# Kernel optimization log

Measured on AMD Instinct MI355X. Metric: run time of the kernel, lower is better.

The kernel has to match this reference:

```python
import jax, jax.numpy as jnp
import numpy as np

RADIUS = 1.3
RES = 256
N_INT = 128
STEP = 0.02


def grid_sample3d(grid, coords):
    # grid: [C, D, H, W]; coords: [N, 3] as (x, y, z) in [-1, 1]
    # trilinear, align_corners=True, border clamp (torch grid_sample semantics)
    D, H, W = grid.shape[1], grid.shape[2], grid.shape[3]

    def to_idx(c, size):
        return jnp.clip((c + 1.0) * 0.5 * (size - 1), 0.0, size - 1.0)

    x = to_idx(coords[:, 0], W)
    y = to_idx(coords[:, 1], H)
    z = to_idx(coords[:, 2], D)
    x0 = jnp.floor(x).astype(jnp.int32)
    y0 = jnp.floor(y).astype(jnp.int32)
    z0 = jnp.floor(z).astype(jnp.int32)
    x1 = jnp.minimum(x0 + 1, W - 1)
    y1 = jnp.minimum(y0 + 1, H - 1)
    z1 = jnp.minimum(z0 + 1, D - 1)
    wx = x - x0.astype(x.dtype)
    wy = y - y0.astype(y.dtype)
    wz = z - z0.astype(z.dtype)

    def g(zi, yi, xi):
        return grid[:, zi, yi, xi]  # [C, N]

    c00 = g(z0, y0, x0) * (1 - wx) + g(z0, y0, x1) * wx
    c01 = g(z0, y1, x0) * (1 - wx) + g(z0, y1, x1) * wx
    c10 = g(z1, y0, x0) * (1 - wx) + g(z1, y0, x1) * wx
    c11 = g(z1, y1, x0) * (1 - wx) + g(z1, y1, x1) * wx
    c0 = c00 * (1 - wy) + c01 * wy
    c1 = c10 * (1 - wy) + c11 * wy
    return (c0 * (1 - wz) + c1 * wz).T  # [N, C]


def sh16(d):
    # real spherical harmonics, degree 4 (instant-ngp / tcnn convention), d unit
    x, y, z = d[:, 0], d[:, 1], d[:, 2]
    xx, yy, zz = x * x, y * y, z * z
    xy, yz, xz = x * y, y * z, x * z
    return jnp.stack([
        jnp.full_like(x, 0.28209479177387814),
        -0.48860251190291987 * y,
        0.48860251190291987 * z,
        -0.48860251190291987 * x,
        1.0925484305920792 * xy,
        -1.0925484305920792 * yz,
        0.94617469575755997 * zz - 0.31539156525251999,
        -1.0925484305920792 * xz,
        0.54627421529603959 * (xx - yy),
        0.59004358992664352 * y * (-3.0 * xx + yy),
        2.8906114426405538 * xy * z,
        0.45704579946446572 * y * (1.0 - 5.0 * zz),
        0.3731763325901154 * z * (5.0 * zz - 3.0),
        0.45704579946446572 * x * (1.0 - 5.0 * zz),
        1.445305721320277 * z * (xx - yy),
        0.59004358992664352 * x * (-xx + 3.0 * yy),
    ], axis=-1)  # [N, 16]


def mlp3(x, W0, W1, W2):
    # FullyFusedMLP: no bias, ReLU hidden, linear output
    h = jnp.maximum(x @ W0, 0.0)
    h = jnp.maximum(h @ W1, 0.0)
    return h @ W2


def setup_inputs() -> dict:
    key = jax.random.key(0)
    k = jax.random.split(key, 10)
    B, FD, NF = 4096, 32, 16
    rays_o = jax.random.normal(k[0], (B, 3), jnp.float32) * 0.5
    rays_d = jax.random.normal(k[1], (B, 3), jnp.float32)
    G1 = jax.random.normal(k[2], (3, RES, RES, RES), jnp.float32) * 0.02
    F = jax.random.normal(k[3], (FD, NF, NF, NF), jnp.float32) * 0.05
    W_sig0 = jax.random.normal(k[4], (FD, 128), jnp.float32) / np.sqrt(FD).astype(np.float32)
    W_sig1 = jax.random.normal(k[5], (128, 128), jnp.float32) / np.float32(np.sqrt(128))
    W_sig2 = jax.random.normal(k[6], (128, 16), jnp.float32) / np.float32(np.sqrt(128))
    W_col0 = jax.random.normal(k[7], (31, 64), jnp.float32) / np.float32(np.sqrt(31))
    W_col1 = jax.random.normal(k[8], (64, 64), jnp.float32) / np.float32(np.sqrt(64))
    W_col2 = jax.random.normal(k[9], (64, 3), jnp.float32) / np.float32(np.sqrt(64))
    return {"rays_o": rays_o, "rays_d": rays_d, "G1": G1, "F": F,
            "W_sig0": W_sig0, "W_sig1": W_sig1, "W_sig2": W_sig2,
            "W_col0": W_col0, "W_col1": W_col1, "W_col2": W_col2}


def reference(rays_o, rays_d, G1, F, W_sig0, W_sig1, W_sig2, W_col0, W_col1, W_col2):
    B = rays_o.shape[0]
    d = rays_d / jnp.linalg.norm(rays_d, axis=-1, keepdims=True)
    # ray-sphere intersection |o + t d| = RADIUS (unit d)
    b = jnp.sum(rays_o * d, axis=-1)
    c = jnp.sum(rays_o * rays_o, axis=-1) - RADIUS ** 2
    disc = b * b - c
    hit = disc > 0
    s = jnp.sqrt(jnp.where(hit, disc, 1.0))
    tmin = jnp.where(hit, jnp.maximum(-b - s, 0.0), 0.0)
    tmax = jnp.where(hit, -b + s, 0.0)
    t = tmin[:, None] + jnp.arange(N_INT + 1, dtype=jnp.float32)[None, :] * STEP  # [B, n+1]
    tmid = 0.5 * (t[:, :-1] + t[:, 1:])  # [B, n]
    mask = hit[:, None] & (tmid <= tmax[:, None])  # [B, n]
    pts = rays_o[:, None, :] + d[:, None, :] * tmid[..., None]  # [B, n, 3]
    coords = (pts / RADIUS).reshape(-1, 3)  # in [-1, 1]
    # hash/indirection lookup: G1 gives learned coords into feature grid F
    g1 = grid_sample3d(G1, coords)        # [N, 3]
    feats = grid_sample3d(F, g1)          # [N, 32]
    sig_out = mlp3(feats, W_sig0, W_sig1, W_sig2)  # [N, 16]
    sigma = jnp.where(mask, sig_out[:, 0].reshape(B, N_INT), 0.0)
    sigma = jnp.maximum(sigma, 0.0)
    pd = jnp.broadcast_to(d[:, None, :], (B, N_INT, 3)).reshape(-1, 3)
    enc = sh16(pd)
    col_raw = mlp3(jnp.concatenate([enc, sig_out[:, 1:]], axis=-1), W_col0, W_col1, W_col2)
    col = jnp.where(mask[..., None], col_raw.reshape(B, N_INT, 3), 0.0)
    # volume rendering (sigma2alpha + shrgb2rgb with white background)
    alpha = 1.0 - jnp.exp(-sigma * STEP)
    T = jnp.cumprod(1.0 - alpha + 1e-10, axis=1)
    T_excl = jnp.concatenate([jnp.ones((B, 1), alpha.dtype), T[:, :-1]], axis=1)
    w = alpha * T_excl
    rgb = jnp.einsum('bn,bnc->bc', w, jax.nn.sigmoid(col))
    rgb = rgb + (1.0 - jnp.sum(w, axis=1, keepdims=True))
    return rgb
```

## Files before the change

kernel.cpp:

```cpp
#include <hip/hip_runtime.h>
#include <stdint.h>

#define STEP 0.02f
#define INV_RADIUS (1.0f/1.3f)
#define RADIUS 1.3f

typedef __bf16   bf16x8 __attribute__((ext_vector_type(8)));
typedef float    f32x4  __attribute__((ext_vector_type(4)));
typedef uint32_t u32x4  __attribute__((ext_vector_type(4)));
typedef uint32_t u32x4a __attribute__((ext_vector_type(4), aligned(8)));

#define FT_OFF   0
#define W0_OFF   262144
#define W1_OFF   270336
#define W2_OFF   303104
#define C0_OFF   307200
#define C1_OFF   311296
#define C2_OFF   319488
#define G1T_OFF  321536
#define WS_NEED  (321536ull + 134217728ull)

#define FE_BYTES  4096
#define SIG_OFF   8192
#define COL_OFF   8704
#define BLOCK_LDS 10752

__device__ __forceinline__ uint32_t pack2(float a, float b){
    uint32_t ua = __float_as_uint(a); ua += 0x7FFFu + ((ua>>16)&1u);
    uint32_t ub = __float_as_uint(b); ub += 0x7FFFu + ((ub>>16)&1u);
    return (ua>>16) | (ub & 0xFFFF0000u);
}
__device__ __forceinline__ float bfl(uint32_t u){ return __uint_as_float(u << 16); }
__device__ __forceinline__ float bfh(uint32_t u){ return __uint_as_float(u & 0xFFFF0000u); }
__device__ __forceinline__ void toidx(float c, float sizem1, int isize,
                                      int& i0, int& i1, float& w){
    float t = (c + 1.f) * 0.5f * sizem1;
    t = fminf(fmaxf(t, 0.f), sizem1);
    float f = floorf(t);
    i0 = (int)f;
    i1 = i0 + 1; if (i1 > isize - 1) i1 = isize - 1;
    w = t - f;
}
__device__ __forceinline__ void lds_fence(){
    asm volatile("s_waitcnt lgkmcnt(0)" ::: "memory");
}
__device__ __forceinline__ uint32_t cvtpk(float lo, float hi){
    uint32_t r;
    asm("v_cvt_pk_bf16_f32 %0, %1, %2" : "=v"(r) : "v"(lo), "v"(hi));
    return r;
}
__device__ __forceinline__ void p32swap(uint32_t& a, uint32_t& b){
    asm("v_permlane32_swap_b32 %0, %1" : "+v"(a), "+v"(b));
}
__device__ __forceinline__ void p16swap(uint32_t& a, uint32_t& b){
    asm("v_permlane16_swap_b32 %0, %1" : "+v"(a), "+v"(b));
}
__device__ __forceinline__ uint32_t pkrelu(float a, float b){
    return cvtpk(fmaxf(a, 0.f), fmaxf(b, 0.f));
}
__device__ __forceinline__ bf16x8 frag_from(uint32_t a, uint32_t b, uint32_t c, uint32_t d){
    union { u32x4 u; bf16x8 h; } cv;
    cv.u = (u32x4){a, b, c, d};
    return cv.h;
}
__device__ __forceinline__ bf16x8 xpose4(const f32x4& t0, const f32x4& t1){
    uint32_t A = pkrelu(t0[0], t0[1]);
    uint32_t B = pkrelu(t0[2], t0[3]);
    uint32_t C = pkrelu(t1[0], t1[1]);
    uint32_t D = pkrelu(t1[2], t1[3]);
    p32swap(A, C); p16swap(A, C);
    p32swap(B, D); p16swap(B, D);
    return frag_from(A, B, C, D);
}
__device__ __forceinline__ void rowlerp(const u32x4a d, bool xe, float wx,
                                        float& v0, float& v1, float& v2){
    uint32_t a01 = xe ? d[2] : d[0];
    uint32_t a2w = xe ? d[3] : d[1];
    float a0 = bfl(a01), a1 = bfh(a01), a2 = bfl(a2w);
    float b0 = bfl(d[2]), b1 = bfh(d[2]), b2 = bfl(d[3]);
    v0 = a0 + (b0 - a0)*wx;
    v1 = a1 + (b1 - a1)*wx;
    v2 = a2 + (b2 - a2)*wx;
}

__global__ __launch_bounds__(256) void prep_g1(const float* __restrict__ G1, uint32_t* __restrict__ dst){
    int idx2 = (blockIdx.x*256 + threadIdx.x)*2;
    float2 a = *(const float2*)(G1 + idx2);
    float2 b = *(const float2*)(G1 + idx2 + 16777216);
    float2 c = *(const float2*)(G1 + idx2 + 33554432);
    uint4 o = make_uint4(pack2(a.x, b.x), pack2(c.x, 0.f),
                         pack2(a.y, b.y), pack2(c.y, 0.f));
    *(uint4*)(dst + idx2*2) = o;
}

__global__ __launch_bounds__(256) void prep_f(const float* __restrict__ F, uint32_t* __restrict__ ws){
    int idx = blockIdx.x * 256 + threadIdx.x;
    if (idx >= 4096) return;
    uint32_t o[16];
    #pragma unroll
    for (int c = 0; c < 16; c++){
        float a = F[(2*c  )*4096 + idx];
        float b = F[(2*c+1)*4096 + idx];
        o[c] = pack2(a, b);
    }
    uint4* dst = (uint4*)ws;
    #pragma unroll
    for (int q = 0; q < 4; q++)
        dst[idx*4 + q] = make_uint4(o[q*4], o[q*4+1], o[q*4+2], o[q*4+3]);
}

__global__ __launch_bounds__(256) void prep_w(const float* __restrict__ W0, const float* __restrict__ W1,
                                              const float* __restrict__ W2, const float* __restrict__ Wc0,
                                              const float* __restrict__ Wc1, const float* __restrict__ Wc2,
                                              char* __restrict__ ws){
    int gid = blockIdx.x * 256 + threadIdx.x;
    if (gid >= 58*64) return;
    int cg = gid >> 6, lane = gid & 63;
    const float* src; int K, N, base_cg, dstoff;
    if      (cg < 8)  { src = W0;  K = 32;  N = 128; base_cg = 0;  dstoff = W0_OFF; }
    else if (cg < 40) { src = W1;  K = 128; N = 128; base_cg = 8;  dstoff = W1_OFF; }
    else if (cg < 44) { src = W2;  K = 128; N = 16;  base_cg = 40; dstoff = W2_OFF; }
    else if (cg < 48) { src = Wc0; K = 31;  N = 64;  base_cg = 44; dstoff = C0_OFF; }
    else if (cg < 56) { src = Wc1; K = 64;  N = 64;  base_cg = 48; dstoff = C1_OFF; }
    else              { src = Wc2; K = 64;  N = 3;   base_cg = 56; dstoff = C2_OFF; }
    bool c0remap = (cg >= 44 && cg < 48);
    int local = cg - base_cg;
    int NT = (N + 15) >> 4;
    int nt = local % NT, kk = local / NT;
    int n = nt*16 + (lane & 15);
    int kbase = kk*32 + (lane >> 4)*8;
    uint32_t o[4];
    #pragma unroll
    for (int jj = 0; jj < 4; jj++){
        int k0 = kbase + jj*2, k1 = k0 + 1;
        int k0s = (c0remap && k0 > 16) ? k0 - 1 : k0;
        int k1s = (c0remap && k1 > 16) ? k1 - 1 : k1;
        bool v0 = (n < N) && (k0s < K) && !(c0remap && k0 == 16);
        bool v1 = (n < N) && (k1s < K) && !(c0remap && k1 == 16);
        float a = v0 ? src[k0s*N + n] : 0.f;
        float b = v1 ? src[k1s*N + n] : 0.f;
        o[jj] = pack2(a, b);
    }
    uint4* dst = (uint4*)(ws + dstoff);
    dst[local*64 + lane] = make_uint4(o[0], o[1], o[2], o[3]);
}

template<bool G1PACK>
__global__ __launch_bounds__(128, 2)
void nerf_fused(const float* __restrict__ rays_o, const float* __restrict__ rays_d,
                const float* __restrict__ G1, const char* __restrict__ ws,
                float* __restrict__ out){
    __shared__ __align__(16) char smem[BLOCK_LDS];
    const int tid  = threadIdx.x;
    const int wv   = tid >> 6;
    const int lane = tid & 63;
    const int nl   = lane & 15;
    const int quad = lane >> 4;
    const int ray  = blockIdx.x;
    char*  FEB  = smem + wv*FE_BYTES;
    float* SIGf = (float*)(smem + SIG_OFF);
    float* COLf = (float*)(smem + COL_OFF);

    float ox = rays_o[ray*3+0], oy = rays_o[ray*3+1], oz = rays_o[ray*3+2];
    float rx = rays_d[ray*3+0], ry = rays_d[ray*3+1], rz = rays_d[ray*3+2];
    float nrm = sqrtf(rx*rx + ry*ry + rz*rz);
    float dx = rx/nrm, dy = ry/nrm, dz = rz/nrm;
    float bq = ox*dx + oy*dy + oz*dz;
    float cq = ox*ox + oy*oy + oz*oz - RADIUS*RADIUS;
    float disc = bq*bq - cq;
    bool  hit = disc > 0.f;
    float sq   = sqrtf(hit ? disc : 1.f);
    float tmin = hit ? fmaxf(-bq - sq, 0.f) : 0.f;
    float tmax = hit ? (-bq + sq) : 0.f;

    uint32_t encw0, encw1, encw2, encw3, cinmask;
    {
        float xx=dx*dx, yy=dy*dy, zz=dz*dz, xy=dx*dy, yz=dy*dz, xz=dx*dz;
        float sh0 = 0.28209479177387814f;
        float sh1 = -0.48860251190291987f*dy;
        float sh2 =  0.48860251190291987f*dz;
        float sh3 = -0.48860251190291987f*dx;
        float sh4 =  1.0925484305920792f*xy;
        float sh5 = -1.0925484305920792f*yz;
        float sh6 =  0.94617469575756f*zz - 0.31539156525252f;
        float sh7 = -1.0925484305920792f*xz;
        float sh8 =  0.5462742152960396f*(xx-yy);
        float sh9 =  0.5900435899266435f*dy*(-3.f*xx+yy);
        float sh10 = 2.890611442640554f*xy*dz;
        float sh11 = 0.4570457994644657f*dy*(1.f-5.f*zz);
        float sh12 = 0.3731763325901154f*dz*(5.f*zz-3.f);
        float sh13 = 0.4570457994644657f*dx*(1.f-5.f*zz);
        float sh14 = 1.445305721320277f*dz*(xx-yy);
        float sh15 = 0.5900435899266435f*dx*(-xx+3.f*yy);
        bool q0 = (quad == 0);
        encw0 = q0 ? pack2(sh0, sh1) : pack2(sh8,  sh9);
        encw1 = q0 ? pack2(sh2, sh3) : pack2(sh10, sh11);
        encw2 = q0 ? pack2(sh4, sh5) : pack2(sh12, sh13);
        encw3 = q0 ? pack2(sh6, sh7) : pack2(sh14, sh15);
        cinmask = (quad == 2) ? 0xFFFF0000u : 0xFFFFFFFFu;
    }

    const char* pW0 = ws + W0_OFF; const char* pW1 = ws + W1_OFF; const char* pW2 = ws + W2_OFF;
    const char* pC0 = ws + C0_OFF; const char* pC1 = ws + C1_OFF; const char* pC2 = ws + C2_OFF;
    const f32x4 vzero = {0.f, 0.f, 0.f, 0.f};

    #define RD_A(bp, linRow, m) \
        (*(const bf16x8*)((bp) + (linRow)*64 + ((quad ^ (((m)>>1)&3))*16)))
    #define LD_B(base, kk, NT, nt) \
        (*(const bf16x8*)((base) + (((kk)*(NT) + (nt))*64 + lane)*16))

    float Dn = (tmax - tmin) * (1.0f/STEP);
    int nv = (int)fminf(128.f, fmaxf(0.f, floorf(Dn + 0.5f) + 1.f));
    int rem = nv - wv*64;
    if (rem > 64) rem = 64;

    if (rem > 0){
        {
            if (lane < rem){
                int p = wv*64 + lane;
                float tmid = tmin + ((float)p + 0.5f) * STEP;
                float px = (ox + dx*tmid) * INV_RADIUS;
                float py = (oy + dy*tmid) * INV_RADIUS;
                float pz = (oz + dz*tmid) * INV_RADIUS;
                int x0,x1,y0,y1,z0,z1; float wx,wy,wz;
                toidx(px, 255.f, 256, x0, x1, wx);
                toidx(py, 255.f, 256, y0, y1, wy);
                toidx(pz, 255.f, 256, z0, z1, wz);
                float g1v[3];
                if constexpr (G1PACK){
                    const uint32_t* Gt = (const uint32_t*)(ws + G1T_OFF);
                    int xs = (x0 < 255) ? x0 : 254;
                    bool xe = (x0 == 255);
                    int r00 = (z0*256 + y0)*256 + xs, r01 = (z0*256 + y1)*256 + xs;
                    int r10 = (z1*256 + y0)*256 + xs, r11 = (z1*256 + y1)*256 + xs;
                    u32x4a d00 = *(const u32x4a*)(Gt + (size_t)r00*2);
                    u32x4a d01 = *(const u32x4a*)(Gt + (size_t)r01*2);
                    u32x4a d10 = *(const u32x4a*)(Gt + (size_t)r10*2);
                    u32x4a d11 = *(const u32x4a*)(Gt + (size_t)r11*2);
                    float v00x,v00y,v00z, v01x,v01y,v01z, v10x,v10y,v10z, v11x,v11y,v11z;
                    rowlerp(d00, xe, wx, v00x, v00y, v00z);
                    rowlerp(d01, xe, wx, v01x, v01y, v01z);
                    rowlerp(d10, xe, wx, v10x, v10y, v10z);
                    rowlerp(d11, xe, wx, v11x, v11y, v11z);
                    float c0x = v00x + (v01x - v00x)*wy, c1x = v10x + (v11x - v10x)*wy;
                    float c0y = v00y + (v01y - v00y)*wy, c1y = v10y + (v11y - v10y)*wy;
                    float c0z = v00z + (v01z - v00z)*wy, c1z = v10z + (v11z - v10z)*wy;
                    g1v[0] = c0x + (c1x - c0x)*wz;
                    g1v[1] = c0y + (c1y - c0y)*wz;
                    g1v[2] = c0z + (c1z - c0z)*wz;
                } else {
                    #pragma unroll
                    for (int ch = 0; ch < 3; ch++){
                        const float* gp = G1 + ch*16777216;
                        int b00 = (z0*256 + y0)*256, b01 = (z0*256 + y1)*256;
                        int b10 = (z1*256 + y0)*256, b11 = (z1*256 + y1)*256;
                        float c000 = gp[b00+x0], c001 = gp[b00+x1];
                        float c010 = gp[b01+x0], c011 = gp[b01+x1];
                        float c100 = gp[b10+x0], c101 = gp[b10+x1];
                        float c110 = gp[b11+x0], c111 = gp[b11+x1];
                        float c00 = c000 + (c001-c000)*wx;
                        float c01 = c010 + (c011-c010)*wx;
                        float c10 = c100 + (c101-c100)*wx;
                        float c11 = c110 + (c111-c110)*wx;
                        float c0 = c00 + (c01-c00)*wy;
                        float c1 = c10 + (c11-c10)*wy;
                        g1v[ch] = c0 + (c1-c0)*wz;
                    }
                }
                int fx0,fx1,fy0,fy1,fz0,fz1; float fwx,fwy,fwz;
                toidx(g1v[0], 15.f, 16, fx0, fx1, fwx);
                toidx(g1v[1], 15.f, 16, fy0, fy1, fwy);
                toidx(g1v[2], 15.f, 16, fz0, fz1, fwz);
                float feats[32];
                #pragma unroll
                for (int i = 0; i < 32; i++) feats[i] = 0.f;
                const uint4* Ft = (const uint4*)(ws + FT_OFF);
                #pragma unroll 2
                for (int corner = 0; corner < 8; corner++){
                    int cz = (corner>>2)&1, cy = (corner>>1)&1, cx = corner&1;
                    int xi = cx?fx1:fx0, yi = cy?fy1:fy0, zi = cz?fz1:fz0;
                    float w = (cx?fwx:1.f-fwx) * (cy?fwy:1.f-fwy) * (cz?fwz:1.f-fwz);
                    const uint4* cp = Ft + ((zi*16 + yi)*16 + xi)*4;
                    #pragma unroll
                    for (int q = 0; q < 4; q++){
                        uint4 v = cp[q];
                        uint32_t u[4] = {v.x, v.y, v.z, v.w};
                        #pragma unroll
                        for (int e = 0; e < 4; e++){
                            feats[q*8 + e*2    ] += w * __uint_as_float(u[e] << 16);
                            feats[q*8 + e*2 + 1] += w * __uint_as_float(u[e] & 0xFFFF0000u);
                        }
                    }
                }
                int fsw = (lane>>1)&3;
                #pragma unroll
                for (int c = 0; c < 4; c++){
                    uint4 v = make_uint4(pack2(feats[c*8+0], feats[c*8+1]),
                                         pack2(feats[c*8+2], feats[c*8+3]),
                                         pack2(feats[c*8+4], feats[c*8+5]),
                                         pack2(feats[c*8+6], feats[c*8+7]));
                    *(uint4*)(FEB + lane*64 + ((c^fsw)*16)) = v;
                }
            }
        }
        lds_fence();

        bf16x8 bW2[4], bC0[4], bC2[2];
        #pragma unroll
        for (int kk = 0; kk < 4; kk++) bW2[kk] = LD_B(pW2, kk, 1, 0);
        #pragma unroll
        for (int nt = 0; nt < 4; nt++) bC0[nt] = LD_B(pC0, 0, 4, nt);
        #pragma unroll
        for (int kk = 0; kk < 2; kk++) bC2[kk] = LD_B(pC2, kk, 1, 0);

        int mtmax = (rem + 15) >> 4;
        #pragma unroll 1
        for (int mt = 0; mt < mtmax; mt++){
            const int mArow = mt*16 + nl;
            const int tb = wv*64 + mt*16;

            bf16x8 fe = RD_A(FEB, mArow, mArow);
            f32x4 a0[8];
            #pragma unroll
            for (int nt = 0; nt < 8; nt++)
                a0[nt] = __builtin_amdgcn_mfma_f32_16x16x32_bf16(LD_B(pW0,0,8,nt), fe, vzero, 0,0,0);
            bf16x8 h1[4];
            #pragma unroll
            for (int kk = 0; kk < 4; kk++)
                h1[kk] = xpose4(a0[2*kk], a0[2*kk+1]);

            f32x4 a1[8];
            #pragma unroll
            for (int nt = 0; nt < 8; nt++) a1[nt] = vzero;
            #pragma unroll
            for (int kk = 0; kk < 4; kk++)
                #pragma unroll
                for (int nt = 0; nt < 8; nt++)
                    a1[nt] = __builtin_amdgcn_mfma_f32_16x16x32_bf16(LD_B(pW1,kk,8,nt), h1[kk], a1[nt], 0,0,0);
            bf16x8 h2[4];
            #pragma unroll
            for (int kk = 0; kk < 4; kk++)
                h2[kk] = xpose4(a1[2*kk], a1[2*kk+1]);

            f32x4 sacc = vzero;
            #pragma unroll
            for (int kk = 0; kk < 4; kk++)
                sacc = __builtin_amdgcn_mfma_f32_16x16x32_bf16(bW2[kk], h2[kk], sacc, 0,0,0);
            if (quad == 0) SIGf[tb + nl] = sacc[0];

            uint32_t ca = cvtpk(sacc[0], sacc[1]);
            uint32_t cb = cvtpk(sacc[2], sacc[3]);
            p32swap(ca, cb); p16swap(ca, cb);
            uint32_t cw0 = encw0, cw2 = encw2;
            p32swap(cw0, ca);
            p32swap(cw2, cb);
            cw0 &= cinmask;
            uint32_t cw1 = (quad < 2) ? encw1 : ca;
            uint32_t cw3 = (quad < 2) ? encw3 : cb;
            bf16x8 cin = frag_from(cw0, cw1, cw2, cw3);

            f32x4 c0[4];
            #pragma unroll
            for (int nt = 0; nt < 4; nt++)
                c0[nt] = __builtin_amdgcn_mfma_f32_16x16x32_bf16(bC0[nt], cin, vzero, 0,0,0);
            bf16x8 g1[2];
            #pragma unroll
            for (int kk = 0; kk < 2; kk++)
                g1[kk] = xpose4(c0[2*kk], c0[2*kk+1]);

            f32x4 c1[4];
            #pragma unroll
            for (int nt = 0; nt < 4; nt++) c1[nt] = vzero;
            #pragma unroll
            for (int kk = 0; kk < 2; kk++)
                #pragma unroll
                for (int nt = 0; nt < 4; nt++)
                    c1[nt] = __builtin_amdgcn_mfma_f32_16x16x32_bf16(LD_B(pC1,kk,4,nt), g1[kk], c1[nt], 0,0,0);
            bf16x8 g2[2];
            #pragma unroll
            for (int kk = 0; kk < 2; kk++)
                g2[kk] = xpose4(c1[2*kk], c1[2*kk+1]);

            f32x4 cc = vzero;
            #pragma unroll
            for (int kk = 0; kk < 2; kk++)
                cc = __builtin_amdgcn_mfma_f32_16x16x32_bf16(bC2[kk], g2[kk], cc, 0,0,0);
            if (quad == 0){
                *(float2*)(COLf + (tb + nl)*4) = make_float2(cc[0], cc[1]);
                COLf[(tb + nl)*4 + 2] = cc[2];
            }
        }
    }

    __syncthreads();

    if (wv != 0) return;

    float t0 = tmin + ((float)lane + 0.5f) * STEP;
    float t1 = tmin + ((float)(lane + 64) + 0.5f) * STEP;
    bool  m0 = hit && (t0 <= tmax);
    bool  m1 = hit && (t1 <= tmax);
    float sig0 = m0 ? fmaxf(SIGf[lane], 0.f) : 0.f;
    float sig1 = m1 ? fmaxf(SIGf[lane + 64], 0.f) : 0.f;
    float e0 = expf(-sig0 * STEP), e1 = expf(-sig1 * STEP);
    float al0 = 1.f - e0, al1 = 1.f - e1;
    float li0 = logf(e0 + 1e-10f), li1 = logf(e1 + 1e-10f);
    float incl0 = li0, incl1 = li1;
    #pragma unroll
    for (int off = 1; off < 64; off <<= 1){
        float v0 = __shfl_up(incl0, off);
        float v1 = __shfl_up(incl1, off);
        if (lane >= off){ incl0 += v0; incl1 += v1; }
    }
    float tot0 = __shfl(incl0, 63);
    float ex0 = incl0 - li0;
    float ex1 = tot0 + incl1 - li1;
    float w0 = al0 * expf(ex0);
    float w1 = al1 * expf(ex1);
    float cr0 = m0 ? COLf[lane*4+0] : 0.f;
    float cg0 = m0 ? COLf[lane*4+1] : 0.f;
    float cb0 = m0 ? COLf[lane*4+2] : 0.f;
    float cr1 = m1 ? COLf[(lane+64)*4+0] : 0.f;
    float cg1 = m1 ? COLf[(lane+64)*4+1] : 0.f;
    float cb1 = m1 ? COLf[(lane+64)*4+2] : 0.f;
    float r = w0 / (1.f + expf(-cr0)) + w1 / (1.f + expf(-cr1));
    float g = w0 / (1.f + expf(-cg0)) + w1 / (1.f + expf(-cg1));
    float b = w0 / (1.f + expf(-cb0)) + w1 / (1.f + expf(-cb1));
    float wa = w0 + w1;
    #pragma unroll
    for (int off = 32; off > 0; off >>= 1){
        r  += __shfl_xor(r,  off);
        g  += __shfl_xor(g,  off);
        b  += __shfl_xor(b,  off);
        wa += __shfl_xor(wa, off);
    }
    if (lane == 0){
        out[ray*3+0] = r + (1.f - wa);
        out[ray*3+1] = g + (1.f - wa);
        out[ray*3+2] = b + (1.f - wa);
    }
    #undef RD_A
    #undef LD_B
}

extern "C" void kernel_launch(void* const* d_in, const int* in_sizes, int n_in,
                              void* d_out, int out_size, void* d_ws, size_t ws_size,
                              hipStream_t stream){
    const float* rays_o = (const float*)d_in[0];
    const float* rays_d = (const float*)d_in[1];
    const float* G1     = (const float*)d_in[2];
    const float* F      = (const float*)d_in[3];
    bool fast = (ws_size >= WS_NEED);
    if (fast)
        prep_g1<<<32768, 256, 0, stream>>>(G1, (uint32_t*)((char*)d_ws + G1T_OFF));
    prep_f<<<16, 256, 0, stream>>>(F, (uint32_t*)d_ws);
    prep_w<<<15, 256, 0, stream>>>((const float*)d_in[4], (const float*)d_in[5],
                                   (const float*)d_in[6], (const float*)d_in[7],
                                   (const float*)d_in[8], (const float*)d_in[9],
                                   (char*)d_ws);
    if (fast)
        nerf_fused<true><<<4096, 128, 0, stream>>>(rays_o, rays_d, G1, (const char*)d_ws, (float*)d_out);
    else
        nerf_fused<false><<<4096, 128, 0, stream>>>(rays_o, rays_d, G1, (const char*)d_ws, (float*)d_out);
}
```

Before: 384.0 us.

## Merge prep kernels, process two M-tiles per MLP iteration, raise occupancy hint

```diff
diff --git a/kernel.cpp b/kernel.cpp
--- a/kernel.cpp
+++ b/kernel.cpp
@@ -7,6 +7,7 @@
 
 typedef __bf16   bf16x8 __attribute__((ext_vector_type(8)));
 typedef float    f32x4  __attribute__((ext_vector_type(4)));
+typedef float    f32x2  __attribute__((ext_vector_type(2)));
 typedef uint32_t u32x4  __attribute__((ext_vector_type(4)));
 typedef uint32_t u32x4a __attribute__((ext_vector_type(4), aligned(8)));
 
@@ -24,6 +25,9 @@
 #define SIG_OFF   8192
 #define COL_OFF   8704
 #define BLOCK_LDS 10752
+
+#define PRIO1 __builtin_amdgcn_s_setprio(1)
+#define PRIO0 __builtin_amdgcn_s_setprio(0)
 
 __device__ __forceinline__ uint32_t pack2(float a, float b){
     uint32_t ua = __float_as_uint(a); ua += 0x7FFFu + ((ua>>16)&1u);
@@ -83,37 +87,39 @@
     v2 = a2 + (b2 - a2)*wx;
 }
 
-__global__ __launch_bounds__(256) void prep_g1(const float* __restrict__ G1, uint32_t* __restrict__ dst){
-    int idx2 = (blockIdx.x*256 + threadIdx.x)*2;
-    float2 a = *(const float2*)(G1 + idx2);
-    float2 b = *(const float2*)(G1 + idx2 + 16777216);
-    float2 c = *(const float2*)(G1 + idx2 + 33554432);
-    uint4 o = make_uint4(pack2(a.x, b.x), pack2(c.x, 0.f),
-                         pack2(a.y, b.y), pack2(c.y, 0.f));
-    *(uint4*)(dst + idx2*2) = o;
-}
-
-__global__ __launch_bounds__(256) void prep_f(const float* __restrict__ F, uint32_t* __restrict__ ws){
-    int idx = blockIdx.x * 256 + threadIdx.x;
-    if (idx >= 4096) return;
-    uint32_t o[16];
-    #pragma unroll
-    for (int c = 0; c < 16; c++){
-        float a = F[(2*c  )*4096 + idx];
-        float b = F[(2*c+1)*4096 + idx];
-        o[c] = pack2(a, b);
-    }
-    uint4* dst = (uint4*)ws;
-    #pragma unroll
-    for (int q = 0; q < 4; q++)
-        dst[idx*4 + q] = make_uint4(o[q*4], o[q*4+1], o[q*4+2], o[q*4+3]);
-}
-
-__global__ __launch_bounds__(256) void prep_w(const float* __restrict__ W0, const float* __restrict__ W1,
-                                              const float* __restrict__ W2, const float* __restrict__ Wc0,
-                                              const float* __restrict__ Wc1, const float* __restrict__ Wc2,
-                                              char* __restrict__ ws){
-    int gid = blockIdx.x * 256 + threadIdx.x;
+__global__ __launch_bounds__(256)
+void prep_all(const float* __restrict__ G1, const float* __restrict__ F,
+              const float* __restrict__ W0, const float* __restrict__ W1,
+              const float* __restrict__ W2, const float* __restrict__ Wc0,
+              const float* __restrict__ Wc1, const float* __restrict__ Wc2,
+              char* __restrict__ ws, int g1b){
+    int bid = blockIdx.x, tid = threadIdx.x;
+    if (bid < g1b){
+        int idx2 = (bid*256 + tid)*2;
+        f32x2 a = __builtin_nontemporal_load((const f32x2*)(G1 + idx2));
+        f32x2 b = __builtin_nontemporal_load((const f32x2*)(G1 + idx2 + 16777216));
+        f32x2 c = __builtin_nontemporal_load((const f32x2*)(G1 + idx2 + 33554432));
+        uint4 o = make_uint4(pack2(a[0], b[0]), pack2(c[0], 0.f),
+                             pack2(a[1], b[1]), pack2(c[1], 0.f));
+        *(uint4*)((uint32_t*)(ws + G1T_OFF) + idx2*2) = o;
+        return;
+    }
+    if (bid < g1b + 16){
+        int idx = (bid - g1b)*256 + tid;
+        uint32_t o[16];
+        #pragma unroll
+        for (int ch = 0; ch < 16; ch++){
+            float a = F[(2*ch  )*4096 + idx];
+            float b = F[(2*ch+1)*4096 + idx];
+            o[ch] = pack2(a, b);
+        }
+        uint4* dst = (uint4*)(ws + FT_OFF);
+        #pragma unroll
+        for (int q = 0; q < 4; q++)
+            dst[idx*4 + q] = make_uint4(o[q*4], o[q*4+1], o[q*4+2], o[q*4+3]);
+        return;
+    }
+    int gid = (bid - g1b - 16)*256 + tid;
     if (gid >= 58*64) return;
     int cg = gid >> 6, lane = gid & 63;
     const float* src; int K, N, base_cg, dstoff;
@@ -146,7 +152,7 @@
 }
 
 template<bool G1PACK>
-__global__ __launch_bounds__(128, 2)
+__global__ __launch_bounds__(128, 4)
 void nerf_fused(const float* __restrict__ rays_o, const float* __restrict__ rays_d,
                 const float* __restrict__ G1, const char* __restrict__ ws,
                 float* __restrict__ out){
@@ -305,89 +311,139 @@
         }
         lds_fence();
 
-        bf16x8 bW2[4], bC0[4], bC2[2];
-        #pragma unroll
-        for (int kk = 0; kk < 4; kk++) bW2[kk] = LD_B(pW2, kk, 1, 0);
-        #pragma unroll
-        for (int nt = 0; nt < 4; nt++) bC0[nt] = LD_B(pC0, 0, 4, nt);
-        #pragma unroll
-        for (int kk = 0; kk < 2; kk++) bC2[kk] = LD_B(pC2, kk, 1, 0);
-
         int mtmax = (rem + 15) >> 4;
         #pragma unroll 1
-        for (int mt = 0; mt < mtmax; mt++){
-            const int mArow = mt*16 + nl;
-            const int tb = wv*64 + mt*16;
-
-            bf16x8 fe = RD_A(FEB, mArow, mArow);
-            f32x4 a0[8];
-            #pragma unroll
-            for (int nt = 0; nt < 8; nt++)
-                a0[nt] = __builtin_amdgcn_mfma_f32_16x16x32_bf16(LD_B(pW0,0,8,nt), fe, vzero, 0,0,0);
-            bf16x8 h1[4];
-            #pragma unroll
-            for (int kk = 0; kk < 4; kk++)
-                h1[kk] = xpose4(a0[2*kk], a0[2*kk+1]);
-
-            f32x4 a1[8];
-            #pragma unroll
-            for (int nt = 0; nt < 8; nt++) a1[nt] = vzero;
+        for (int mp = 0; mp < mtmax; mp += 2){
+            const int rA = mp*16 + nl;
+            const int rB = rA + 16;
+            const int tbA = wv*64 + mp*16;
+            const int tbB = tbA + 16;
+
+            bf16x8 feA = RD_A(FEB, rA, rA);
+            bf16x8 feB = RD_A(FEB, rB, rB);
+            f32x4 a0A[8], a0B[8];
+            PRIO1;
+            #pragma unroll
+            for (int nt = 0; nt < 8; nt++){
+                bf16x8 w = LD_B(pW0, 0, 8, nt);
+                a0A[nt] = __builtin_amdgcn_mfma_f32_16x16x32_bf16(w, feA, vzero, 0,0,0);
+                a0B[nt] = __builtin_amdgcn_mfma_f32_16x16x32_bf16(w, feB, vzero, 0,0,0);
+            }
+            PRIO0;
+            bf16x8 h1A[4], h1B[4];
+            #pragma unroll
+            for (int kk = 0; kk < 4; kk++){
+                h1A[kk] = xpose4(a0A[2*kk], a0A[2*kk+1]);
+                h1B[kk] = xpose4(a0B[2*kk], a0B[2*kk+1]);
+            }
+
+            f32x4 a1A[8], a1B[8];
+            #pragma unroll
+            for (int nt = 0; nt < 8; nt++){ a1A[nt] = vzero; a1B[nt] = vzero; }
+            PRIO1;
             #pragma unroll
             for (int kk = 0; kk < 4; kk++)
                 #pragma unroll
-                for (int nt = 0; nt < 8; nt++)
-                    a1[nt] = __builtin_amdgcn_mfma_f32_16x16x32_bf16(LD_B(pW1,kk,8,nt), h1[kk], a1[nt], 0,0,0);
-            bf16x8 h2[4];
-            #pragma unroll
-            for (int kk = 0; kk < 4; kk++)
-                h2[kk] = xpose4(a1[2*kk], a1[2*kk+1]);
-
-            f32x4 sacc = vzero;
-            #pragma unroll
-            for (int kk = 0; kk < 4; kk++)
-                sacc = __builtin_amdgcn_mfma_f32_16x16x32_bf16(bW2[kk], h2[kk], sacc, 0,0,0);
-            if (quad == 0) SIGf[tb + nl] = sacc[0];
-
-            uint32_t ca = cvtpk(sacc[0], sacc[1]);
-            uint32_t cb = cvtpk(sacc[2], sacc[3]);
-            p32swap(ca, cb); p16swap(ca, cb);
-            uint32_t cw0 = encw0, cw2 = encw2;
-            p32swap(cw0, ca);
-            p32swap(cw2, cb);
-            cw0 &= cinmask;
-            uint32_t cw1 = (quad < 2) ? encw1 : ca;
-            uint32_t cw3 = (quad < 2) ? encw3 : cb;
-            bf16x8 cin = frag_from(cw0, cw1, cw2, cw3);
-
-            f32x4 c0[4];
-            #pragma unroll
-            for (int nt = 0; nt < 4; nt++)
-                c0[nt] = __builtin_amdgcn_mfma_f32_16x16x32_bf16(bC0[nt], cin, vzero, 0,0,0);
-            bf16x8 g1[2];
-            #pragma unroll
-            for (int kk = 0; kk < 2; kk++)
-                g1[kk] = xpose4(c0[2*kk], c0[2*kk+1]);
-
-            f32x4 c1[4];
-            #pragma unroll
-            for (int nt = 0; nt < 4; nt++) c1[nt] = vzero;
+                for (int nt = 0; nt < 8; nt++){
+                    bf16x8 w = LD_B(pW1, kk, 8, nt);
+                    a1A[nt] = __builtin_amdgcn_mfma_f32_16x16x32_bf16(w, h1A[kk], a1A[nt], 0,0,0);
+                    a1B[nt] = __builtin_amdgcn_mfma_f32_16x16x32_bf16(w, h1B[kk], a1B[nt], 0,0,0);
+                }
+            PRIO0;
+            bf16x8 h2A[4], h2B[4];
+            #pragma unroll
+            for (int kk = 0; kk < 4; kk++){
+                h2A[kk] = xpose4(a1A[2*kk], a1A[2*kk+1]);
+                h2B[kk] = xpose4(a1B[2*kk], a1B[2*kk+1]);
+            }
+
+            f32x4 sA = vzero, sB = vzero;
+            PRIO1;
+            #pragma unroll
+            for (int kk = 0; kk < 4; kk++){
+                bf16x8 w = LD_B(pW2, kk, 1, 0);
+                sA = __builtin_amdgcn_mfma_f32_16x16x32_bf16(w, h2A[kk], sA, 0,0,0);
+                sB = __builtin_amdgcn_mfma_f32_16x16x32_bf16(w, h2B[kk], sB, 0,0,0);
+            }
+            PRIO0;
+            if (quad == 0){ SIGf[tbA + nl] = sA[0]; SIGf[tbB + nl] = sB[0]; }
+
+            bf16x8 cinA, cinB;
+            {
+                uint32_t ca = cvtpk(sA[0], sA[1]);
+                uint32_t cb = cvtpk(sA[2], sA[3]);
+                p32swap(ca, cb); p16swap(ca, cb);
+                uint32_t cw0 = encw0, cw2 = encw2;
+                p32swap(cw0, ca);
+                p32swap(cw2, cb);
+                cw0 &= cinmask;
+                uint32_t cw1 = (quad < 2) ? encw1 : ca;
+                uint32_t cw3 = (quad < 2) ? encw3 : cb;
+                cinA = frag_from(cw0, cw1, cw2, cw3);
+            }
+            {
+                uint32_t ca = cvtpk(sB[0], sB[1]);
+                uint32_t cb = cvtpk(sB[2], sB[3]);
+                p32swap(ca, cb); p16swap(ca, cb);
+                uint32_t cw0 = encw0, cw2 = encw2;
+                p32swap(cw0, ca);
+                p32swap(cw2, cb);
+                cw0 &= cinmask;
+                uint32_t cw1 = (quad < 2) ? encw1 : ca;
+                uint32_t cw3 = (quad < 2) ? encw3 : cb;
+                cinB = frag_from(cw0, cw1, cw2, cw3);
+            }
+
+            f32x4 c0A[4], c0B[4];
+            PRIO1;
+            #pragma unroll
+            for (int nt = 0; nt < 4; nt++){
+                bf16x8 w = LD_B(pC0, 0, 4, nt);
+                c0A[nt] = __builtin_amdgcn_mfma_f32_16x16x32_bf16(w, cinA, vzero, 0,0,0);
+                c0B[nt] = __builtin_amdgcn_mfma_f32_16x16x32_bf16(w, cinB, vzero, 0,0,0);
+            }
+            PRIO0;
+            bf16x8 g1A[2], g1B[2];
+            #pragma unroll
+            for (int kk = 0; kk < 2; kk++){
+                g1A[kk] = xpose4(c0A[2*kk], c0A[2*kk+1]);
+                g1B[kk] = xpose4(c0B[2*kk], c0B[2*kk+1]);
+            }
+
+            f32x4 c1A[4], c1B[4];
+            #pragma unroll
+            for (int nt = 0; nt < 4; nt++){ c1A[nt] = vzero; c1B[nt] = vzero; }
+            PRIO1;
             #pragma unroll
             for (int kk = 0; kk < 2; kk++)
                 #pragma unroll
-                for (int nt = 0; nt < 4; nt++)
-                    c1[nt] = __builtin_amdgcn_mfma_f32_16x16x32_bf16(LD_B(pC1,kk,4,nt), g1[kk], c1[nt], 0,0,0);
-            bf16x8 g2[2];
-            #pragma unroll
-            for (int kk = 0; kk < 2; kk++)
-                g2[kk] = xpose4(c1[2*kk], c1[2*kk+1]);
-
-            f32x4 cc = vzero;
-            #pragma unroll
-            for (int kk = 0; kk < 2; kk++)
-                cc = __builtin_amdgcn_mfma_f32_16x16x32_bf16(bC2[kk], g2[kk], cc, 0,0,0);
+                for (int nt = 0; nt < 4; nt++){
+                    bf16x8 w = LD_B(pC1, kk, 4, nt);
+                    c1A[nt] = __builtin_amdgcn_mfma_f32_16x16x32_bf16(w, g1A[kk], c1A[nt], 0,0,0);
+                    c1B[nt] = __builtin_amdgcn_mfma_f32_16x16x32_bf16(w, g1B[kk], c1B[nt], 0,0,0);
+                }
+            PRIO0;
+            bf16x8 g2A[2], g2B[2];
+            #pragma unroll
+            for (int kk = 0; kk < 2; kk++){
+                g2A[kk] = xpose4(c1A[2*kk], c1A[2*kk+1]);
+                g2B[kk] = xpose4(c1B[2*kk], c1B[2*kk+1]);
+            }
+
+            f32x4 ccA = vzero, ccB = vzero;
+            PRIO1;
+            #pragma unroll
+            for (int kk = 0; kk < 2; kk++){
+                bf16x8 w = LD_B(pC2, kk, 1, 0);
+                ccA = __builtin_amdgcn_mfma_f32_16x16x32_bf16(w, g2A[kk], ccA, 0,0,0);
+                ccB = __builtin_amdgcn_mfma_f32_16x16x32_bf16(w, g2B[kk], ccB, 0,0,0);
+            }
+            PRIO0;
             if (quad == 0){
-                *(float2*)(COLf + (tb + nl)*4) = make_float2(cc[0], cc[1]);
-                COLf[(tb + nl)*4 + 2] = cc[2];
+                *(float2*)(COLf + (tbA + nl)*4) = make_float2(ccA[0], ccA[1]);
+                COLf[(tbA + nl)*4 + 2] = ccA[2];
+                *(float2*)(COLf + (tbB + nl)*4) = make_float2(ccB[0], ccB[1]);
+                COLf[(tbB + nl)*4 + 2] = ccB[2];
             }
         }
     }
@@ -451,13 +507,12 @@
     const float* G1     = (const float*)d_in[2];
     const float* F      = (const float*)d_in[3];
     bool fast = (ws_size >= WS_NEED);
-    if (fast)
-        prep_g1<<<32768, 256, 0, stream>>>(G1, (uint32_t*)((char*)d_ws + G1T_OFF));
-    prep_f<<<16, 256, 0, stream>>>(F, (uint32_t*)d_ws);
-    prep_w<<<15, 256, 0, stream>>>((const float*)d_in[4], (const float*)d_in[5],
-                                   (const float*)d_in[6], (const float*)d_in[7],
-                                   (const float*)d_in[8], (const float*)d_in[9],
-                                   (char*)d_ws);
+    int g1b = fast ? 32768 : 0;
+    prep_all<<<g1b + 31, 256, 0, stream>>>(G1, F,
+                                           (const float*)d_in[4], (const float*)d_in[5],
+                                           (const float*)d_in[6], (const float*)d_in[7],
+                                           (const float*)d_in[8], (const float*)d_in[9],
+                                           (char*)d_ws, g1b);
     if (fast)
         nerf_fused<true><<<4096, 128, 0, stream>>>(rays_o, rays_d, G1, (const char*)d_ws, (float*)d_out);
     else
```

After: 437.8 us. 1.14x slower.
